# Kernel optimization log

Hardware: AMD Instinct MI355X
Metric: run time of the kernel (lower is better)

The kernel has to match this reference:

```python
import jax, jax.numpy as jnp
import numpy as np

HIDDEN = 2048
INTER = 1408
N_ROUTED = 32
N_SHARED = 2
TOP_K = 6
B, S = 2, 1024


def setup_inputs() -> dict:
    key = jax.random.key(0)
    ks = jax.random.split(key, 9)
    scale = 0.02
    x = jax.random.normal(ks[0], (B, S, HIDDEN), dtype=jnp.float32)
    w_router = jax.random.normal(ks[1], (HIDDEN, N_ROUTED), dtype=jnp.float32) * scale
    wg = jax.random.normal(ks[2], (N_ROUTED, HIDDEN, INTER), dtype=jnp.float32) * scale
    wu = jax.random.normal(ks[3], (N_ROUTED, HIDDEN, INTER), dtype=jnp.float32) * scale
    wd = jax.random.normal(ks[4], (N_ROUTED, INTER, HIDDEN), dtype=jnp.float32) * scale
    sg = jax.random.normal(ks[5], (N_SHARED, HIDDEN, INTER), dtype=jnp.float32) * scale
    su = jax.random.normal(ks[6], (N_SHARED, HIDDEN, INTER), dtype=jnp.float32) * scale
    sd = jax.random.normal(ks[7], (N_SHARED, INTER, HIDDEN), dtype=jnp.float32) * scale
    return {"x": x, "w_router": w_router, "wg": wg, "wu": wu, "wd": wd,
            "sg": sg, "su": su, "sd": sd}


def _swiglu(xf, wg_e, wu_e, wd_e):
    # xf: [T, D]; wg_e/wu_e: [D, F]; wd_e: [F, D]
    h = jax.nn.silu(xf @ wg_e) * (xf @ wu_e)
    return h @ wd_e


def reference(x, w_router, wg, wu, wd, sg, su, sd):
    Bb, Ss, D = x.shape
    xf = x.reshape(-1, D)                      # [T, D], T = B*S
    T = xf.shape[0]

    # Shared experts: applied densely to every token, summed.
    shared = jnp.zeros_like(xf)
    for i in range(sg.shape[0]):               # small fixed count (2)
        shared = shared + _swiglu(xf, sg[i], su[i], sd[i])

    # Router: softmax over all routed experts, then top-k + renormalize.
    probs = jax.nn.softmax(xf @ w_router, axis=-1)            # [T, E]
    topw, topi = jax.lax.top_k(probs, TOP_K)                  # [T, K]
    topw = topw / jnp.sum(topw, axis=-1, keepdims=True)

    # Dense [T, E] combine weights (zero where expert not selected).
    E = wg.shape[0]
    wdense = jnp.zeros((T, E), dtype=xf.dtype)
    wdense = wdense.at[jnp.arange(T)[:, None], topi].add(topw)

    # Scan over experts, accumulating weighted expert outputs (memory-light).
    def body(acc, ew):
        wg_e, wu_e, wd_e, w_e = ew            # w_e: [T] combine weight for this expert
        y = _swiglu(xf, wg_e, wu_e, wd_e)     # [T, D]
        return acc + w_e[:, None] * y, None

    routed, _ = jax.lax.scan(body, jnp.zeros_like(xf), (wg, wu, wd, wdense.T))

    return (shared + routed).reshape(Bb, Ss, D)
```

## Files before the change

kernel.cpp:

```cpp
#include <hip/hip_runtime.h>
#include <hip/hip_bf16.h>

#define T_TOK 2048
#define D_HID 2048
#define F_INT 1408
#define N_EXP 32
#define TOPK 6
#define NJOBS 34
#define SH_BASE 12288
#define ROWS_TOTAL 16384
#define BM 128
#define MAXT 159
#define LDSW 40

typedef __bf16 bf16;
typedef __bf16 bf16x4 __attribute__((ext_vector_type(4)));
typedef __bf16 bf16x8 __attribute__((ext_vector_type(8)));
typedef float f32x4 __attribute__((ext_vector_type(4)));

__device__ __forceinline__ int swz(int r, int k) {
    return r * LDSW + (((k >> 2) ^ ((r >> 2) & 7)) << 2) + (k & 3);
}

__device__ __forceinline__ int decode_tile(const int* __restrict__ counts, int bid, int NBN,
                                           int& job, int& n0, int& m0) {
    int total = 0;
    for (int j = 0; j < NJOBS; ++j) {
        int c = (j < N_EXP) ? counts[j] : T_TOK;
        total += ((c + BM - 1) >> 7) * NBN;
    }
    if (bid >= total) return 0;
    int q = total >> 3, r = total & 7, x = bid & 7, o = bid >> 3;
    int L = (x < r ? x * (q + 1) : r * (q + 1) + (x - r) * q) + o;
    int acc = 0;
    for (int j = 0; j < NJOBS; ++j) {
        int c = (j < N_EXP) ? counts[j] : T_TOK;
        int tc = (c + BM - 1) >> 7;
        int b = tc * NBN;
        if (L < acc + b) {
            int rem = L - acc;
            int n0i = rem / tc;
            job = j;
            n0 = n0i << 7;
            m0 = (rem - n0i * tc) << 7;
            return 1;
        }
        acc += b;
    }
    return 0;
}

__global__ __launch_bounds__(256) void k_router(const float* __restrict__ x,
                                                const float* __restrict__ wr,
                                                int* __restrict__ counts,
                                                int* __restrict__ tok_e,
                                                float* __restrict__ tok_w) {
    int t = blockIdx.x;
    int tid = threadIdx.x;
    __shared__ float xs[D_HID];
    __shared__ float part[8][32];
    __shared__ float probs[N_EXP];

    const float4* xsrc = (const float4*)(x + (size_t)t * D_HID);
    float4* xdst = (float4*)xs;
    for (int i = tid; i < D_HID / 4; i += 256) xdst[i] = xsrc[i];
    __syncthreads();

    int e = tid & 31, c = tid >> 5;
    float p = 0.f;
    const float* wp = wr + e;
    #pragma unroll 8
    for (int h = c * 256; h < c * 256 + 256; ++h) p += xs[h] * wp[h * 32];
    part[c][e] = p;
    __syncthreads();

    if (tid < 32) {
        float l = 0.f;
        #pragma unroll
        for (int cc = 0; cc < 8; ++cc) l += part[cc][tid];
        float m = l;
        for (int off = 16; off; off >>= 1) m = fmaxf(m, __shfl_xor(m, off));
        float ex = __expf(l - m);
        float s = ex;
        for (int off = 16; off; off >>= 1) s += __shfl_xor(s, off);
        probs[tid] = ex / s;
    }
    __syncthreads();

    if (tid == 0) {
        unsigned used = 0;
        int ids[TOPK]; float wsv[TOPK]; float wsum = 0.f;
        for (int k = 0; k < TOPK; ++k) {
            int best = 0; float bv = -1.f;
            for (int ee = 0; ee < N_EXP; ++ee)
                if (!((used >> ee) & 1u) && probs[ee] > bv) { bv = probs[ee]; best = ee; }
            used |= 1u << best;
            ids[k] = best; wsv[k] = bv; wsum += bv;
        }
        float inv = 1.f / wsum;
        for (int k = 0; k < TOPK; ++k) {
            tok_e[t * TOPK + k] = ids[k];
            tok_w[t * TOPK + k] = wsv[k] * inv;
            atomicAdd(&counts[ids[k]], 1);
        }
    }
}

__global__ void k_plan(const int* __restrict__ counts, int* __restrict__ offs,
                       int* __restrict__ cursors) {
    int tid = threadIdx.x;
    if (tid < N_EXP) cursors[tid] = 0;
    if (tid == 0) {
        int o = 0;
        offs[0] = 0;
        for (int e2 = 0; e2 < N_EXP; ++e2) { o += counts[e2]; offs[e2 + 1] = o; }
        offs[33] = offs[32] + T_TOK;
        offs[34] = offs[33] + T_TOK;
    }
}

__global__ __launch_bounds__(256) void k_assign(const int* __restrict__ tok_e,
                                                const int* __restrict__ offs,
                                                int* __restrict__ cursors,
                                                int* __restrict__ slots,
                                                int* __restrict__ rowtok) {
    int t = blockIdx.x * 256 + threadIdx.x;
    #pragma unroll
    for (int k = 0; k < TOPK; ++k) {
        int e = tok_e[t * TOPK + k];
        int pos = atomicAdd(&cursors[e], 1);
        int slot = offs[e] + pos;
        slots[t * TOPK + k] = slot;
        rowtok[slot] = t;
    }
    rowtok[SH_BASE + t] = t;
    rowtok[SH_BASE + T_TOK + t] = t;
}

__global__ __launch_bounds__(256, 2) void k_gateup(
    const float* __restrict__ x, const float* __restrict__ wg, const float* __restrict__ wu,
    const float* __restrict__ sg, const float* __restrict__ su,
    const int* __restrict__ rowtok, const int* __restrict__ counts, const int* __restrict__ offs,
    bf16* __restrict__ H) {

    int job, n0, m0;
    if (!decode_tile(counts, blockIdx.x, F_INT / 128, job, n0, m0)) return;
    int cnt = (job < N_EXP) ? counts[job] : T_TOK;
    int base = offs[job];
    const float* Wg = (job < N_EXP) ? wg + (size_t)job * D_HID * F_INT
                                    : sg + (size_t)(job - N_EXP) * D_HID * F_INT;
    const float* Wu = (job < N_EXP) ? wu + (size_t)job * D_HID * F_INT
                                    : su + (size_t)(job - N_EXP) * D_HID * F_INT;

    __shared__ bf16 As[128 * LDSW];
    __shared__ bf16 Bg[128 * LDSW];
    __shared__ bf16 Bu[128 * LDSW];

    int tid = threadIdx.x;
    int lane = tid & 63;
    int wid = tid >> 6;
    int wm = (wid >> 1) * 64;
    int wn = (wid & 1) * 64;

    int ar = tid >> 1;
    int akh = (tid & 1) * 16;
    int grow_a = m0 + ar; if (grow_a > cnt - 1) grow_a = cnt - 1;
    const float* asrc = x + (size_t)rowtok[base + grow_a] * D_HID + akh;

    int k4 = (tid >> 5) * 4;
    int nn = (tid & 31) * 4;
    const float* gsrc = Wg + (size_t)k4 * F_INT + n0 + nn;
    const float* usrc = Wu + (size_t)k4 * F_INT + n0 + nn;

    f32x4 accg[4][4], accu[4][4];
    f32x4 zero = {0.f, 0.f, 0.f, 0.f};
    #pragma unroll
    for (int i = 0; i < 4; ++i)
        #pragma unroll
        for (int j = 0; j < 4; ++j) { accg[i][j] = zero; accu[i][j] = zero; }

    float4 a_r[4], g_r[4], u_r[4];

    auto LOAD = [&](int k0) {
        const float4* s4 = (const float4*)(asrc + k0);
        a_r[0] = s4[0]; a_r[1] = s4[1]; a_r[2] = s4[2]; a_r[3] = s4[3];
        const float* g0 = gsrc + (size_t)k0 * F_INT;
        g_r[0] = *(const float4*)g0;
        g_r[1] = *(const float4*)(g0 + F_INT);
        g_r[2] = *(const float4*)(g0 + 2 * F_INT);
        g_r[3] = *(const float4*)(g0 + 3 * F_INT);
        const float* u0 = usrc + (size_t)k0 * F_INT;
        u_r[0] = *(const float4*)u0;
        u_r[1] = *(const float4*)(u0 + F_INT);
        u_r[2] = *(const float4*)(u0 + 2 * F_INT);
        u_r[3] = *(const float4*)(u0 + 3 * F_INT);
    };

    auto WRITE = [&]() {
        #pragma unroll
        for (int q = 0; q < 4; ++q) {
            float4 f = a_r[q];
            bf16x4 v = {(bf16)f.x, (bf16)f.y, (bf16)f.z, (bf16)f.w};
            *(bf16x4*)&As[swz(ar, akh + 4 * q)] = v;
        }
        bf16x4 p0 = {(bf16)g_r[0].x, (bf16)g_r[1].x, (bf16)g_r[2].x, (bf16)g_r[3].x};
        bf16x4 p1 = {(bf16)g_r[0].y, (bf16)g_r[1].y, (bf16)g_r[2].y, (bf16)g_r[3].y};
        bf16x4 p2 = {(bf16)g_r[0].z, (bf16)g_r[1].z, (bf16)g_r[2].z, (bf16)g_r[3].z};
        bf16x4 p3 = {(bf16)g_r[0].w, (bf16)g_r[1].w, (bf16)g_r[2].w, (bf16)g_r[3].w};
        *(bf16x4*)&Bg[swz(nn + 0, k4)] = p0;
        *(bf16x4*)&Bg[swz(nn + 1, k4)] = p1;
        *(bf16x4*)&Bg[swz(nn + 2, k4)] = p2;
        *(bf16x4*)&Bg[swz(nn + 3, k4)] = p3;
        bf16x4 q0 = {(bf16)u_r[0].x, (bf16)u_r[1].x, (bf16)u_r[2].x, (bf16)u_r[3].x};
        bf16x4 q1 = {(bf16)u_r[0].y, (bf16)u_r[1].y, (bf16)u_r[2].y, (bf16)u_r[3].y};
        bf16x4 q2 = {(bf16)u_r[0].z, (bf16)u_r[1].z, (bf16)u_r[2].z, (bf16)u_r[3].z};
        bf16x4 q3 = {(bf16)u_r[0].w, (bf16)u_r[1].w, (bf16)u_r[2].w, (bf16)u_r[3].w};
        *(bf16x4*)&Bu[swz(nn + 0, k4)] = q0;
        *(bf16x4*)&Bu[swz(nn + 1, k4)] = q1;
        *(bf16x4*)&Bu[swz(nn + 2, k4)] = q2;
        *(bf16x4*)&Bu[swz(nn + 3, k4)] = q3;
    };

    const int NT = D_HID / 32;
    LOAD(0);
    for (int kt = 0; kt < NT; ++kt) {
        WRITE();
        __syncthreads();
        if (kt + 1 < NT) LOAD((kt + 1) * 32);

        int kk = (lane >> 4) * 8;
        bf16x8 af[4];
        #pragma unroll
        for (int mf = 0; mf < 4; ++mf) {
            int R = wm + mf * 16 + (lane & 15);
            bf16x4 lo = *(const bf16x4*)&As[swz(R, kk)];
            bf16x4 hi = *(const bf16x4*)&As[swz(R, kk + 4)];
            af[mf] = __builtin_shufflevector(lo, hi, 0, 1, 2, 3, 4, 5, 6, 7);
        }
        #pragma unroll
        for (int nf = 0; nf < 4; ++nf) {
            int rn = wn + nf * 16 + (lane & 15);
            int o0 = swz(rn, kk), o1 = swz(rn, kk + 4);
            bf16x4 bl = *(const bf16x4*)&Bg[o0];
            bf16x4 bh = *(const bf16x4*)&Bg[o1];
            bf16x8 bfr = __builtin_shufflevector(bl, bh, 0, 1, 2, 3, 4, 5, 6, 7);
            bf16x4 ul = *(const bf16x4*)&Bu[o0];
            bf16x4 uh = *(const bf16x4*)&Bu[o1];
            bf16x8 ufr = __builtin_shufflevector(ul, uh, 0, 1, 2, 3, 4, 5, 6, 7);
            #pragma unroll
            for (int mf = 0; mf < 4; ++mf) {
                accg[mf][nf] = __builtin_amdgcn_mfma_f32_16x16x32_bf16(af[mf], bfr, accg[mf][nf], 0, 0, 0);
                accu[mf][nf] = __builtin_amdgcn_mfma_f32_16x16x32_bf16(af[mf], ufr, accu[mf][nf], 0, 0, 0);
            }
        }
        asm volatile("s_barrier" ::: "memory");
    }

    #pragma unroll
    for (int mf = 0; mf < 4; ++mf) {
        #pragma unroll
        for (int nf = 0; nf < 4; ++nf) {
            int col = n0 + wn + nf * 16 + (lane & 15);
            #pragma unroll
            for (int r = 0; r < 4; ++r) {
                int grow = m0 + wm + mf * 16 + (lane >> 4) * 4 + r;
                if (grow < cnt) {
                    float g = accg[mf][nf][r];
                    float u = accu[mf][nf][r];
                    float h = g * u / (1.f + __expf(-g));
                    H[(size_t)(base + grow) * F_INT + col] = (bf16)h;
                }
            }
        }
    }
}

__global__ __launch_bounds__(256, 2) void k_down(
    const bf16* __restrict__ H, const float* __restrict__ wd, const float* __restrict__ sd,
    const int* __restrict__ counts, const int* __restrict__ offs,
    bf16* __restrict__ P) {

    int job, n0, m0;
    if (!decode_tile(counts, blockIdx.x, D_HID / 128, job, n0, m0)) return;
    int cnt = (job < N_EXP) ? counts[job] : T_TOK;
    int base = offs[job];
    const float* Wd = (job < N_EXP) ? wd + (size_t)job * F_INT * D_HID
                                    : sd + (size_t)(job - N_EXP) * F_INT * D_HID;

    __shared__ bf16 As[128 * LDSW];
    __shared__ bf16 Bs[128 * LDSW];

    int tid = threadIdx.x;
    int lane = tid & 63;
    int wid = tid >> 6;
    int wm = (wid >> 1) * 64;
    int wn = (wid & 1) * 64;

    int ar = tid >> 1;
    int akh = (tid & 1) * 16;
    int grow_a = m0 + ar; if (grow_a > cnt - 1) grow_a = cnt - 1;
    const bf16* asrc = H + (size_t)(base + grow_a) * F_INT + akh;

    int k4 = (tid >> 5) * 4;
    int nn = (tid & 31) * 4;
    const float* bsrc = Wd + (size_t)k4 * D_HID + n0 + nn;

    f32x4 acc[4][4];
    f32x4 zero = {0.f, 0.f, 0.f, 0.f};
    #pragma unroll
    for (int i = 0; i < 4; ++i)
        #pragma unroll
        for (int j = 0; j < 4; ++j) acc[i][j] = zero;

    bf16x8 h_r[2];
    float4 b_r[4];

    auto LOAD = [&](int k0) {
        h_r[0] = *(const bf16x8*)(asrc + k0);
        h_r[1] = *(const bf16x8*)(asrc + k0 + 8);
        const float* b0 = bsrc + (size_t)k0 * D_HID;
        b_r[0] = *(const float4*)b0;
        b_r[1] = *(const float4*)(b0 + D_HID);
        b_r[2] = *(const float4*)(b0 + 2 * D_HID);
        b_r[3] = *(const float4*)(b0 + 3 * D_HID);
    };

    auto WRITE = [&]() {
        bf16x4 w0 = __builtin_shufflevector(h_r[0], h_r[0], 0, 1, 2, 3);
        bf16x4 w1 = __builtin_shufflevector(h_r[0], h_r[0], 4, 5, 6, 7);
        bf16x4 w2 = __builtin_shufflevector(h_r[1], h_r[1], 0, 1, 2, 3);
        bf16x4 w3 = __builtin_shufflevector(h_r[1], h_r[1], 4, 5, 6, 7);
        *(bf16x4*)&As[swz(ar, akh + 0)]  = w0;
        *(bf16x4*)&As[swz(ar, akh + 4)]  = w1;
        *(bf16x4*)&As[swz(ar, akh + 8)]  = w2;
        *(bf16x4*)&As[swz(ar, akh + 12)] = w3;
        bf16x4 p0 = {(bf16)b_r[0].x, (bf16)b_r[1].x, (bf16)b_r[2].x, (bf16)b_r[3].x};
        bf16x4 p1 = {(bf16)b_r[0].y, (bf16)b_r[1].y, (bf16)b_r[2].y, (bf16)b_r[3].y};
        bf16x4 p2 = {(bf16)b_r[0].z, (bf16)b_r[1].z, (bf16)b_r[2].z, (bf16)b_r[3].z};
        bf16x4 p3 = {(bf16)b_r[0].w, (bf16)b_r[1].w, (bf16)b_r[2].w, (bf16)b_r[3].w};
        *(bf16x4*)&Bs[swz(nn + 0, k4)] = p0;
        *(bf16x4*)&Bs[swz(nn + 1, k4)] = p1;
        *(bf16x4*)&Bs[swz(nn + 2, k4)] = p2;
        *(bf16x4*)&Bs[swz(nn + 3, k4)] = p3;
    };

    const int NT = F_INT / 32;
    LOAD(0);
    for (int kt = 0; kt < NT; ++kt) {
        WRITE();
        __syncthreads();
        if (kt + 1 < NT) LOAD((kt + 1) * 32);

        int kk = (lane >> 4) * 8;
        bf16x8 af[4];
        #pragma unroll
        for (int mf = 0; mf < 4; ++mf) {
            int R = wm + mf * 16 + (lane & 15);
            bf16x4 lo = *(const bf16x4*)&As[swz(R, kk)];
            bf16x4 hi = *(const bf16x4*)&As[swz(R, kk + 4)];
            af[mf] = __builtin_shufflevector(lo, hi, 0, 1, 2, 3, 4, 5, 6, 7);
        }
        #pragma unroll
        for (int nf = 0; nf < 4; ++nf) {
            int rn = wn + nf * 16 + (lane & 15);
            bf16x4 bl = *(const bf16x4*)&Bs[swz(rn, kk)];
            bf16x4 bh = *(const bf16x4*)&Bs[swz(rn, kk + 4)];
            bf16x8 bfr = __builtin_shufflevector(bl, bh, 0, 1, 2, 3, 4, 5, 6, 7);
            #pragma unroll
            for (int mf = 0; mf < 4; ++mf)
                acc[mf][nf] = __builtin_amdgcn_mfma_f32_16x16x32_bf16(af[mf], bfr, acc[mf][nf], 0, 0, 0);
        }
        asm volatile("s_barrier" ::: "memory");
    }

    #pragma unroll
    for (int mf = 0; mf < 4; ++mf) {
        #pragma unroll
        for (int nf = 0; nf < 4; ++nf) {
            int col = n0 + wn + nf * 16 + (lane & 15);
            #pragma unroll
            for (int r = 0; r < 4; ++r) {
                int grow = m0 + wm + mf * 16 + (lane >> 4) * 4 + r;
                if (grow < cnt)
                    P[(size_t)(base + grow) * D_HID + col] = (bf16)acc[mf][nf][r];
            }
        }
    }
}

__global__ __launch_bounds__(256) void k_combine(const bf16* __restrict__ P,
                                                 const int* __restrict__ slots,
                                                 const float* __restrict__ tok_w,
                                                 float* __restrict__ out) {
    int t = blockIdx.x;
    int tid = threadIdx.x;
    __shared__ int ss[TOPK];
    __shared__ float ww[TOPK];
    if (tid < TOPK) { ss[tid] = slots[t * TOPK + tid]; ww[tid] = tok_w[t * TOPK + tid]; }
    __syncthreads();
    int c0 = tid * 8;
    float acc[8];
    {
        bf16x8 v0 = *(const bf16x8*)(P + (size_t)(SH_BASE + t) * D_HID + c0);
        bf16x8 v1 = *(const bf16x8*)(P + (size_t)(SH_BASE + T_TOK + t) * D_HID + c0);
        #pragma unroll
        for (int i = 0; i < 8; ++i) acc[i] = (float)v0[i] + (float)v1[i];
    }
    #pragma unroll
    for (int k = 0; k < TOPK; ++k) {
        bf16x8 v = *(const bf16x8*)(P + (size_t)ss[k] * D_HID + c0);
        float w = ww[k];
        #pragma unroll
        for (int i = 0; i < 8; ++i) acc[i] += w * (float)v[i];
    }
    float4 o0 = {acc[0], acc[1], acc[2], acc[3]};
    float4 o1 = {acc[4], acc[5], acc[6], acc[7]};
    *(float4*)(out + (size_t)t * D_HID + c0) = o0;
    *(float4*)(out + (size_t)t * D_HID + c0 + 4) = o1;
}

extern "C" void kernel_launch(void* const* d_in, const int* in_sizes, int n_in,
                              void* d_out, int out_size, void* d_ws, size_t ws_size,
                              hipStream_t stream) {
    const float* x  = (const float*)d_in[0];
    const float* wr = (const float*)d_in[1];
    const float* wg = (const float*)d_in[2];
    const float* wu = (const float*)d_in[3];
    const float* wd = (const float*)d_in[4];
    const float* sg = (const float*)d_in[5];
    const float* su = (const float*)d_in[6];
    const float* sd = (const float*)d_in[7];
    float* out = (float*)d_out;

    char* w = (char*)d_ws;
    int*   counts   = (int*)(w + 0);
    int*   cursors  = (int*)(w + 256);
    int*   offs     = (int*)(w + 512);
    int*   tok_e    = (int*)(w + 8192);
    float* tok_w    = (float*)(w + 8192 + 49152);
    int*   slots    = (int*)(w + 8192 + 2 * 49152);
    int*   rowtok   = (int*)(w + 8192 + 3 * 49152);
    bf16*  H        = (bf16*)(w + 262144);
    bf16*  P        = (bf16*)(w + 262144 + (size_t)ROWS_TOTAL * F_INT * 2);

    hipMemsetAsync(counts, 0, 128, stream);
    k_router<<<T_TOK, 256, 0, stream>>>(x, wr, counts, tok_e, tok_w);
    k_plan<<<1, 64, 0, stream>>>(counts, offs, cursors);
    k_assign<<<T_TOK / 256, 256, 0, stream>>>(tok_e, offs, cursors, slots, rowtok);
    k_gateup<<<MAXT * (F_INT / 128), 256, 0, stream>>>(
        x, wg, wu, sg, su, rowtok, counts, offs, H);
    k_down<<<MAXT * (D_HID / 128), 256, 0, stream>>>(
        H, wd, sd, counts, offs, P);
    k_combine<<<T_TOK, 256, 0, stream>>>(P, slots, tok_w, out);
}
```

Measured before the change: 854.1 us.

## Double-buffer LDS in gate/up and down GEMMs, shrink gate/up M tile to 64

Both grouped GEMM kernels move to double-buffered shared memory tiles, so the next K slice is written while the current one feeds the MFMAs, with one barrier per iteration instead of two. The gate/up kernel's M tile drops from 128 to 64 rows, which raises the tile count and cuts accumulator registers, and both kernels request 3 blocks per CU. The aim is to hide global-load and LDS-write latency and improve occupancy. The cost is more shared memory per block, and the smaller tile rereads the gate/up weights twice as often.

```diff
diff --git a/kernel.cpp b/kernel.cpp
--- a/kernel.cpp
+++ b/kernel.cpp
@@ -9,8 +9,8 @@
 #define NJOBS 34
 #define SH_BASE 12288
 #define ROWS_TOTAL 16384
-#define BM 128
-#define MAXT 159
+#define MAXT_GU 288
+#define MAXT_DN 159
 #define LDSW 40
 
 typedef __bf16 bf16;
@@ -18,16 +18,19 @@
 typedef __bf16 bf16x8 __attribute__((ext_vector_type(8)));
 typedef float f32x4 __attribute__((ext_vector_type(4)));
 
+#define BAR() asm volatile("s_waitcnt lgkmcnt(0)\n\ts_barrier" ::: "memory")
+
 __device__ __forceinline__ int swz(int r, int k) {
     return r * LDSW + (((k >> 2) ^ ((r >> 2) & 7)) << 2) + (k & 3);
 }
 
-__device__ __forceinline__ int decode_tile(const int* __restrict__ counts, int bid, int NBN,
+__device__ __forceinline__ int decode_tile(const int* __restrict__ counts, int bid,
+                                           int NBN, int MSH, int NSH,
                                            int& job, int& n0, int& m0) {
     int total = 0;
     for (int j = 0; j < NJOBS; ++j) {
         int c = (j < N_EXP) ? counts[j] : T_TOK;
-        total += ((c + BM - 1) >> 7) * NBN;
+        total += ((c + (1 << MSH) - 1) >> MSH) * NBN;
     }
     if (bid >= total) return 0;
     int q = total >> 3, r = total & 7, x = bid & 7, o = bid >> 3;
@@ -35,14 +38,14 @@
     int acc = 0;
     for (int j = 0; j < NJOBS; ++j) {
         int c = (j < N_EXP) ? counts[j] : T_TOK;
-        int tc = (c + BM - 1) >> 7;
+        int tc = (c + (1 << MSH) - 1) >> MSH;
         int b = tc * NBN;
         if (L < acc + b) {
             int rem = L - acc;
             int n0i = rem / tc;
             job = j;
-            n0 = n0i << 7;
-            m0 = (rem - n0i * tc) << 7;
+            n0 = n0i << NSH;
+            m0 = (rem - n0i * tc) << MSH;
             return 1;
         }
         acc += b;
@@ -137,14 +140,14 @@
     rowtok[SH_BASE + T_TOK + t] = t;
 }
 
-__global__ __launch_bounds__(256, 2) void k_gateup(
+__global__ __launch_bounds__(256, 3) void k_gateup(
     const float* __restrict__ x, const float* __restrict__ wg, const float* __restrict__ wu,
     const float* __restrict__ sg, const float* __restrict__ su,
     const int* __restrict__ rowtok, const int* __restrict__ counts, const int* __restrict__ offs,
     bf16* __restrict__ H) {
 
     int job, n0, m0;
-    if (!decode_tile(counts, blockIdx.x, F_INT / 128, job, n0, m0)) return;
+    if (!decode_tile(counts, blockIdx.x, F_INT / 128, 6, 7, job, n0, m0)) return;
     int cnt = (job < N_EXP) ? counts[job] : T_TOK;
     int base = offs[job];
     const float* Wg = (job < N_EXP) ? wg + (size_t)job * D_HID * F_INT
@@ -152,18 +155,18 @@
     const float* Wu = (job < N_EXP) ? wu + (size_t)job * D_HID * F_INT
                                     : su + (size_t)(job - N_EXP) * D_HID * F_INT;
 
-    __shared__ bf16 As[128 * LDSW];
-    __shared__ bf16 Bg[128 * LDSW];
-    __shared__ bf16 Bu[128 * LDSW];
+    __shared__ bf16 As[2][64 * LDSW];
+    __shared__ bf16 Bg[2][128 * LDSW];
+    __shared__ bf16 Bu[2][128 * LDSW];
 
     int tid = threadIdx.x;
     int lane = tid & 63;
     int wid = tid >> 6;
-    int wm = (wid >> 1) * 64;
+    int wm = (wid >> 1) * 32;
     int wn = (wid & 1) * 64;
 
-    int ar = tid >> 1;
-    int akh = (tid & 1) * 16;
+    int ar = tid >> 2;
+    int akh = (tid & 3) * 8;
     int grow_a = m0 + ar; if (grow_a > cnt - 1) grow_a = cnt - 1;
     const float* asrc = x + (size_t)rowtok[base + grow_a] * D_HID + akh;
 
@@ -172,18 +175,18 @@
     const float* gsrc = Wg + (size_t)k4 * F_INT + n0 + nn;
     const float* usrc = Wu + (size_t)k4 * F_INT + n0 + nn;
 
-    f32x4 accg[4][4], accu[4][4];
+    f32x4 accg[2][4], accu[2][4];
     f32x4 zero = {0.f, 0.f, 0.f, 0.f};
     #pragma unroll
-    for (int i = 0; i < 4; ++i)
+    for (int i = 0; i < 2; ++i)
         #pragma unroll
         for (int j = 0; j < 4; ++j) { accg[i][j] = zero; accu[i][j] = zero; }
 
-    float4 a_r[4], g_r[4], u_r[4];
+    float4 a_r[2], g_r[4], u_r[4];
 
     auto LOAD = [&](int k0) {
         const float4* s4 = (const float4*)(asrc + k0);
-        a_r[0] = s4[0]; a_r[1] = s4[1]; a_r[2] = s4[2]; a_r[3] = s4[3];
+        a_r[0] = s4[0]; a_r[1] = s4[1];
         const float* g0 = gsrc + (size_t)k0 * F_INT;
         g_r[0] = *(const float4*)g0;
         g_r[1] = *(const float4*)(g0 + F_INT);
@@ -196,68 +199,72 @@
         u_r[3] = *(const float4*)(u0 + 3 * F_INT);
     };
 
-    auto WRITE = [&]() {
-        #pragma unroll
-        for (int q = 0; q < 4; ++q) {
+    auto WRITE = [&](int s) {
+        #pragma unroll
+        for (int q = 0; q < 2; ++q) {
             float4 f = a_r[q];
             bf16x4 v = {(bf16)f.x, (bf16)f.y, (bf16)f.z, (bf16)f.w};
-            *(bf16x4*)&As[swz(ar, akh + 4 * q)] = v;
+            *(bf16x4*)&As[s][swz(ar, akh + 4 * q)] = v;
         }
         bf16x4 p0 = {(bf16)g_r[0].x, (bf16)g_r[1].x, (bf16)g_r[2].x, (bf16)g_r[3].x};
         bf16x4 p1 = {(bf16)g_r[0].y, (bf16)g_r[1].y, (bf16)g_r[2].y, (bf16)g_r[3].y};
         bf16x4 p2 = {(bf16)g_r[0].z, (bf16)g_r[1].z, (bf16)g_r[2].z, (bf16)g_r[3].z};
         bf16x4 p3 = {(bf16)g_r[0].w, (bf16)g_r[1].w, (bf16)g_r[2].w, (bf16)g_r[3].w};
-        *(bf16x4*)&Bg[swz(nn + 0, k4)] = p0;
-        *(bf16x4*)&Bg[swz(nn + 1, k4)] = p1;
-        *(bf16x4*)&Bg[swz(nn + 2, k4)] = p2;
-        *(bf16x4*)&Bg[swz(nn + 3, k4)] = p3;
+        *(bf16x4*)&Bg[s][swz(nn + 0, k4)] = p0;
+        *(bf16x4*)&Bg[s][swz(nn + 1, k4)] = p1;
+        *(bf16x4*)&Bg[s][swz(nn + 2, k4)] = p2;
+        *(bf16x4*)&Bg[s][swz(nn + 3, k4)] = p3;
         bf16x4 q0 = {(bf16)u_r[0].x, (bf16)u_r[1].x, (bf16)u_r[2].x, (bf16)u_r[3].x};
         bf16x4 q1 = {(bf16)u_r[0].y, (bf16)u_r[1].y, (bf16)u_r[2].y, (bf16)u_r[3].y};
         bf16x4 q2 = {(bf16)u_r[0].z, (bf16)u_r[1].z, (bf16)u_r[2].z, (bf16)u_r[3].z};
         bf16x4 q3 = {(bf16)u_r[0].w, (bf16)u_r[1].w, (bf16)u_r[2].w, (bf16)u_r[3].w};
-        *(bf16x4*)&Bu[swz(nn + 0, k4)] = q0;
-        *(bf16x4*)&Bu[swz(nn + 1, k4)] = q1;
-        *(bf16x4*)&Bu[swz(nn + 2, k4)] = q2;
-        *(bf16x4*)&Bu[swz(nn + 3, k4)] = q3;
+        *(bf16x4*)&Bu[s][swz(nn + 0, k4)] = q0;
+        *(bf16x4*)&Bu[s][swz(nn + 1, k4)] = q1;
+        *(bf16x4*)&Bu[s][swz(nn + 2, k4)] = q2;
+        *(bf16x4*)&Bu[s][swz(nn + 3, k4)] = q3;
     };
 
     const int NT = D_HID / 32;
     LOAD(0);
+    WRITE(0);
+    LOAD(32);
+    BAR();
+
     for (int kt = 0; kt < NT; ++kt) {
-        WRITE();
-        __syncthreads();
-        if (kt + 1 < NT) LOAD((kt + 1) * 32);
+        int cur = kt & 1;
+        if (kt + 1 < NT) WRITE(cur ^ 1);
+        if (kt + 2 < NT) LOAD((kt + 2) * 32);
 
         int kk = (lane >> 4) * 8;
-        bf16x8 af[4];
-        #pragma unroll
-        for (int mf = 0; mf < 4; ++mf) {
+        bf16x8 af[2];
+        #pragma unroll
+        for (int mf = 0; mf < 2; ++mf) {
             int R = wm + mf * 16 + (lane & 15);
-            bf16x4 lo = *(const bf16x4*)&As[swz(R, kk)];
-            bf16x4 hi = *(const bf16x4*)&As[swz(R, kk + 4)];
+            bf16x4 lo = *(const bf16x4*)&As[cur][swz(R, kk)];
+            bf16x4 hi = *(const bf16x4*)&As[cur][swz(R, kk + 4)];
             af[mf] = __builtin_shufflevector(lo, hi, 0, 1, 2, 3, 4, 5, 6, 7);
         }
         #pragma unroll
         for (int nf = 0; nf < 4; ++nf) {
             int rn = wn + nf * 16 + (lane & 15);
             int o0 = swz(rn, kk), o1 = swz(rn, kk + 4);
-            bf16x4 bl = *(const bf16x4*)&Bg[o0];
-            bf16x4 bh = *(const bf16x4*)&Bg[o1];
+            bf16x4 bl = *(const bf16x4*)&Bg[cur][o0];
+            bf16x4 bh = *(const bf16x4*)&Bg[cur][o1];
             bf16x8 bfr = __builtin_shufflevector(bl, bh, 0, 1, 2, 3, 4, 5, 6, 7);
-            bf16x4 ul = *(const bf16x4*)&Bu[o0];
-            bf16x4 uh = *(const bf16x4*)&Bu[o1];
+            bf16x4 ul = *(const bf16x4*)&Bu[cur][o0];
+            bf16x4 uh = *(const bf16x4*)&Bu[cur][o1];
             bf16x8 ufr = __builtin_shufflevector(ul, uh, 0, 1, 2, 3, 4, 5, 6, 7);
             #pragma unroll
-            for (int mf = 0; mf < 4; ++mf) {
+            for (int mf = 0; mf < 2; ++mf) {
                 accg[mf][nf] = __builtin_amdgcn_mfma_f32_16x16x32_bf16(af[mf], bfr, accg[mf][nf], 0, 0, 0);
                 accu[mf][nf] = __builtin_amdgcn_mfma_f32_16x16x32_bf16(af[mf], ufr, accu[mf][nf], 0, 0, 0);
             }
         }
-        asm volatile("s_barrier" ::: "memory");
-    }
-
-    #pragma unroll
-    for (int mf = 0; mf < 4; ++mf) {
+        BAR();
+    }
+
+    #pragma unroll
+    for (int mf = 0; mf < 2; ++mf) {
         #pragma unroll
         for (int nf = 0; nf < 4; ++nf) {
             int col = n0 + wn + nf * 16 + (lane & 15);
@@ -275,20 +282,20 @@
     }
 }
 
-__global__ __launch_bounds__(256, 2) void k_down(
+__global__ __launch_bounds__(256, 3) void k_down(
     const bf16* __restrict__ H, const float* __restrict__ wd, const float* __restrict__ sd,
     const int* __restrict__ counts, const int* __restrict__ offs,
     bf16* __restrict__ P) {
 
     int job, n0, m0;
-    if (!decode_tile(counts, blockIdx.x, D_HID / 128, job, n0, m0)) return;
+    if (!decode_tile(counts, blockIdx.x, D_HID / 128, 7, 7, job, n0, m0)) return;
     int cnt = (job < N_EXP) ? counts[job] : T_TOK;
     int base = offs[job];
     const float* Wd = (job < N_EXP) ? wd + (size_t)job * F_INT * D_HID
                                     : sd + (size_t)(job - N_EXP) * F_INT * D_HID;
 
-    __shared__ bf16 As[128 * LDSW];
-    __shared__ bf16 Bs[128 * LDSW];
+    __shared__ bf16 As[2][128 * LDSW];
+    __shared__ bf16 Bs[2][128 * LDSW];
 
     int tid = threadIdx.x;
     int lane = tid & 63;
@@ -325,52 +332,56 @@
         b_r[3] = *(const float4*)(b0 + 3 * D_HID);
     };
 
-    auto WRITE = [&]() {
+    auto WRITE = [&](int s) {
         bf16x4 w0 = __builtin_shufflevector(h_r[0], h_r[0], 0, 1, 2, 3);
         bf16x4 w1 = __builtin_shufflevector(h_r[0], h_r[0], 4, 5, 6, 7);
         bf16x4 w2 = __builtin_shufflevector(h_r[1], h_r[1], 0, 1, 2, 3);
         bf16x4 w3 = __builtin_shufflevector(h_r[1], h_r[1], 4, 5, 6, 7);
-        *(bf16x4*)&As[swz(ar, akh + 0)]  = w0;
-        *(bf16x4*)&As[swz(ar, akh + 4)]  = w1;
-        *(bf16x4*)&As[swz(ar, akh + 8)]  = w2;
-        *(bf16x4*)&As[swz(ar, akh + 12)] = w3;
+        *(bf16x4*)&As[s][swz(ar, akh + 0)]  = w0;
+        *(bf16x4*)&As[s][swz(ar, akh + 4)]  = w1;
+        *(bf16x4*)&As[s][swz(ar, akh + 8)]  = w2;
+        *(bf16x4*)&As[s][swz(ar, akh + 12)] = w3;
         bf16x4 p0 = {(bf16)b_r[0].x, (bf16)b_r[1].x, (bf16)b_r[2].x, (bf16)b_r[3].x};
         bf16x4 p1 = {(bf16)b_r[0].y, (bf16)b_r[1].y, (bf16)b_r[2].y, (bf16)b_r[3].y};
         bf16x4 p2 = {(bf16)b_r[0].z, (bf16)b_r[1].z, (bf16)b_r[2].z, (bf16)b_r[3].z};
         bf16x4 p3 = {(bf16)b_r[0].w, (bf16)b_r[1].w, (bf16)b_r[2].w, (bf16)b_r[3].w};
-        *(bf16x4*)&Bs[swz(nn + 0, k4)] = p0;
-        *(bf16x4*)&Bs[swz(nn + 1, k4)] = p1;
-        *(bf16x4*)&Bs[swz(nn + 2, k4)] = p2;
-        *(bf16x4*)&Bs[swz(nn + 3, k4)] = p3;
+        *(bf16x4*)&Bs[s][swz(nn + 0, k4)] = p0;
+        *(bf16x4*)&Bs[s][swz(nn + 1, k4)] = p1;
+        *(bf16x4*)&Bs[s][swz(nn + 2, k4)] = p2;
+        *(bf16x4*)&Bs[s][swz(nn + 3, k4)] = p3;
     };
 
     const int NT = F_INT / 32;
     LOAD(0);
+    WRITE(0);
+    LOAD(32);
+    BAR();
+
     for (int kt = 0; kt < NT; ++kt) {
-        WRITE();
-        __syncthreads();
-        if (kt + 1 < NT) LOAD((kt + 1) * 32);
+        int cur = kt & 1;
+        if (kt + 1 < NT) WRITE(cur ^ 1);
+        if (kt + 2 < NT) LOAD((kt + 2) * 32);
 
         int kk = (lane >> 4) * 8;
         bf16x8 af[4];
         #pragma unroll
         for (int mf = 0; mf < 4; ++mf) {
             int R = wm + mf * 16 + (lane & 15);
-            bf16x4 lo = *(const bf16x4*)&As[swz(R, kk)];
-            bf16x4 hi = *(const bf16x4*)&As[swz(R, kk + 4)];
+            bf16x4 lo = *(const bf16x4*)&As[cur][swz(R, kk)];
+            bf16x4 hi = *(const bf16x4*)&As[cur][swz(R, kk + 4)];
             af[mf] = __builtin_shufflevector(lo, hi, 0, 1, 2, 3, 4, 5, 6, 7);
         }
         #pragma unroll
         for (int nf = 0; nf < 4; ++nf) {
             int rn = wn + nf * 16 + (lane & 15);
-            bf16x4 bl = *(const bf16x4*)&Bs[swz(rn, kk)];
-            bf16x4 bh = *(const bf16x4*)&Bs[swz(rn, kk + 4)];
+            bf16x4 bl = *(const bf16x4*)&Bs[cur][swz(rn, kk)];
+            bf16x4 bh = *(const bf16x4*)&Bs[cur][swz(rn, kk + 4)];
             bf16x8 bfr = __builtin_shufflevector(bl, bh, 0, 1, 2, 3, 4, 5, 6, 7);
             #pragma unroll
             for (int mf = 0; mf < 4; ++mf)
                 acc[mf][nf] = __builtin_amdgcn_mfma_f32_16x16x32_bf16(af[mf], bfr, acc[mf][nf], 0, 0, 0);
         }
-        asm volatile("s_barrier" ::: "memory");
+        BAR();
     }
 
     #pragma unroll
@@ -447,9 +458,9 @@
     k_router<<<T_TOK, 256, 0, stream>>>(x, wr, counts, tok_e, tok_w);
     k_plan<<<1, 64, 0, stream>>>(counts, offs, cursors);
     k_assign<<<T_TOK / 256, 256, 0, stream>>>(tok_e, offs, cursors, slots, rowtok);
-    k_gateup<<<MAXT * (F_INT / 128), 256, 0, stream>>>(
+    k_gateup<<<MAXT_GU * (F_INT / 128), 256, 0, stream>>>(
         x, wg, wu, sg, su, rowtok, counts, offs, H);
-    k_down<<<MAXT * (D_HID / 128), 256, 0, stream>>>(
+    k_down<<<MAXT_DN * (D_HID / 128), 256, 0, stream>>>(
         H, wd, sd, counts, offs, P);
     k_combine<<<T_TOK, 256, 0, stream>>>(P, slots, tok_w, out);
 }
```

Measured after the change: 811.4 us. -5.0%, faster.
